# Kernel tuning notes

Hardware: AMD Instinct MI355X
Metric: run time of the kernel (lower is better)

The kernel has to match this reference:

```python
import jax, jax.numpy as jnp
import numpy as np

N, FEATS, CLASSES, E = 100000, 32, 16, 1600000
EMB_DIM = 1 + int(np.log2(FEATS))  # 6
HIDDEN = 3 + EMB_DIM               # 9
DEPTH = 10
DIFF = 0.9


def setup_inputs() -> dict:
    key = jax.random.key(0)
    ks = jax.random.split(key, 10)
    s = lambda k, *sh: jax.random.normal(k, sh, dtype=jnp.float32)
    return {
        "x": s(ks[0], N, FEATS),
        "edges": jax.random.randint(ks[1], (2, E), 0, N, dtype=jnp.int64),
        "emb_table": s(ks[2], FEATS, EMB_DIM) * 0.1,
        "W1": s(ks[3], 1 + EMB_DIM, HIDDEN) * 0.3,
        "b1": jnp.zeros((HIDDEN,), jnp.float32),
        "W2": s(ks[4], HIDDEN, 1) * 0.3,
        "b2": jnp.zeros((1,), jnp.float32),
        "Wout": s(ks[5], FEATS, CLASSES) * 0.1,
        "bout": jnp.zeros((CLASSES,), jnp.float32),
    }


def reference(x, edges, emb_table, W1, b1, W2, b2, Wout, bout):
    n, f = x.shape
    src, dst = edges[0], edges[1]
    # symmetric degree normalization (parameter-free GraphConv)
    deg = jax.ops.segment_sum(jnp.ones((src.shape[0],), x.dtype), dst, num_segments=n)
    deg = jnp.maximum(deg, 1.0)
    norm = jax.lax.rsqrt(deg[src] * deg[dst])  # [E]

    def conv(h):
        return jax.ops.segment_sum(h[src] * norm[:, None], dst, num_segments=n)

    def diffuse(h):
        h0 = h
        for _ in range(DEPTH):
            h = conv(h) * DIFF + (1.0 - DIFF) * h0
        return h

    x = diffuse(x)
    # per-(node, class) MLP: x.t().reshape(-1,1) orders rows class-major
    col = x.T.reshape(-1, 1)                       # [f*n, 1]
    emb = jnp.repeat(emb_table, n, axis=0)         # [f*n, EMB_DIM] (class cl repeated n times)
    h = jnp.concatenate([col, emb], axis=1)        # [f*n, 1+EMB_DIM]
    h = jax.nn.relu(h @ W1 + b1)
    h = h @ W2 + b2                                # [f*n, 1]
    x = h.reshape(f, n).T                          # [n, f]
    x = diffuse(x)
    return x @ Wout + bout
```

## Files before the change

### kernel.cpp

```cpp
#include <hip/hip_runtime.h>
#include <hip/hip_fp16.h>

#define ELL_CAP 64
#define NSLICE 8
#define EPB 2048


__global__ __launch_bounds__(256) void ell_fill(
    const int* __restrict__ edges, int* __restrict__ deg,
    int* __restrict__ ell, int e, int n, int slice_sz) {
    int slice = blockIdx.x & (NSLICE - 1);
    int chunk = blockIdx.x >> 3;
    int lo = slice * slice_sz;
    int hi = min(n, lo + slice_sz);
    int base = chunk * EPB + threadIdx.x;
#pragma unroll
    for (int k = 0; k < EPB / 256; ++k) {
        int i = base + k * 256;
        if (i >= e) break;
        int d = __builtin_nontemporal_load(&edges[e + i]);
        if (d < lo || d >= hi) continue;
        int s = __builtin_nontemporal_load(&edges[i]);
        int slot = atomicAdd(&deg[d], 1);
        if (slot < ELL_CAP) ell[((size_t)d << 6) + slot] = s;
    }
}

__global__ void nodeconst_kernel(const int* __restrict__ deg, float* __restrict__ rs,
                                 float* __restrict__ sq, float* __restrict__ wdeg,
                                 int* __restrict__ ell, int n) {
    int i = blockIdx.x * blockDim.x + threadIdx.x;
    if (i > n) return;
    int v = (i < n) ? deg[i] : 0;
    float d = (float)max(v, 1);
    float r = rsqrtf(d);
    rs[i] = r;
    sq[i] = sqrtf(d);
    wdeg[i] = 0.9f * r * r;
    if (i < n) {
        int dg = min(v, ELL_CAP);
        int dgp = (dg + 7) & ~7;
        for (int k = dg; k < dgp; ++k) ell[((size_t)i << 6) + k] = n;
    }
}

__global__ void prescale_kernel(const float2* __restrict__ x2, const float* __restrict__ rs,
                                __half2* __restrict__ g, int n) {
    int i = blockIdx.x * blockDim.x + threadIdx.x;
    int node = i >> 4;
    if (node > n) return;
    if (node == n) { g[i] = __floats2half2_rn(0.f, 0.f); return; }
    float2 v = x2[i];
    float r = rs[node];
    g[i] = __floats2half2_rn(v.x * r, v.y * r);
}


union H4 {
    uint2 u;
    __half2 h[2];
};

__global__ __launch_bounds__(256) void conv_kernel(
    const uint2* __restrict__ gin, const uint2* __restrict__ g0,
    uint2* __restrict__ gout, const int* __restrict__ deg,
    const int* __restrict__ ell, const float* __restrict__ wdeg, int n) {
    int gid = blockIdx.x * blockDim.x + threadIdx.x;
    int node = gid >> 3;
    int q = gid & 7;
    if (node > n) return;
    int dg = (node < n) ? min(deg[node], ELL_CAP) : 0;
    int dgp = (dg + 7) & ~7;
    int j0 = node << 6;
    int jend = j0 + dgp;
    float w = wdeg[node];
    H4 g0v;
    g0v.u = g0[gid];
    float ax0 = 0.f, ay0 = 0.f, az0 = 0.f, aw0 = 0.f;
    float ax1 = 0.f, ay1 = 0.f, az1 = 0.f, aw1 = 0.f;
    float ax2 = 0.f, ay2 = 0.f, az2 = 0.f, aw2 = 0.f;
    float ax3 = 0.f, ay3 = 0.f, az3 = 0.f, aw3 = 0.f;
    int scur = ell[j0 + q];
    for (int j = j0; j < jend; j += 8) {
        int snext = ell[j + 8 + q];
        int s0 = __shfl(scur, 0, 8), s1 = __shfl(scur, 1, 8);
        int s2 = __shfl(scur, 2, 8), s3 = __shfl(scur, 3, 8);
        int s4 = __shfl(scur, 4, 8), s5 = __shfl(scur, 5, 8);
        int s6 = __shfl(scur, 6, 8), s7 = __shfl(scur, 7, 8);
        H4 v0, v1, v2, v3, v4, v5, v6, v7;
        v0.u = gin[(size_t)s0 * 8 + q];
        v1.u = gin[(size_t)s1 * 8 + q];
        v2.u = gin[(size_t)s2 * 8 + q];
        v3.u = gin[(size_t)s3 * 8 + q];
        v4.u = gin[(size_t)s4 * 8 + q];
        v5.u = gin[(size_t)s5 * 8 + q];
        v6.u = gin[(size_t)s6 * 8 + q];
        v7.u = gin[(size_t)s7 * 8 + q];
        float2 lo, hi;
        lo = __half22float2(v0.h[0]); hi = __half22float2(v0.h[1]);
        ax0 += lo.x; ay0 += lo.y; az0 += hi.x; aw0 += hi.y;
        lo = __half22float2(v1.h[0]); hi = __half22float2(v1.h[1]);
        ax1 += lo.x; ay1 += lo.y; az1 += hi.x; aw1 += hi.y;
        lo = __half22float2(v2.h[0]); hi = __half22float2(v2.h[1]);
        ax2 += lo.x; ay2 += lo.y; az2 += hi.x; aw2 += hi.y;
        lo = __half22float2(v3.h[0]); hi = __half22float2(v3.h[1]);
        ax3 += lo.x; ay3 += lo.y; az3 += hi.x; aw3 += hi.y;
        lo = __half22float2(v4.h[0]); hi = __half22float2(v4.h[1]);
        ax0 += lo.x; ay0 += lo.y; az0 += hi.x; aw0 += hi.y;
        lo = __half22float2(v5.h[0]); hi = __half22float2(v5.h[1]);
        ax1 += lo.x; ay1 += lo.y; az1 += hi.x; aw1 += hi.y;
        lo = __half22float2(v6.h[0]); hi = __half22float2(v6.h[1]);
        ax2 += lo.x; ay2 += lo.y; az2 += hi.x; aw2 += hi.y;
        lo = __half22float2(v7.h[0]); hi = __half22float2(v7.h[1]);
        ax3 += lo.x; ay3 += lo.y; az3 += hi.x; aw3 += hi.y;
        scur = snext;
    }
    float2 g0lo = __half22float2(g0v.h[0]);
    float2 g0hi = __half22float2(g0v.h[1]);
    float rx = w * (ax0 + ax1 + ax2 + ax3) + 0.1f * g0lo.x;
    float ry = w * (ay0 + ay1 + ay2 + ay3) + 0.1f * g0lo.y;
    float rz = w * (az0 + az1 + az2 + az3) + 0.1f * g0hi.x;
    float rw = w * (aw0 + aw1 + aw2 + aw3) + 0.1f * g0hi.y;
    H4 o;
    o.h[0] = __floats2half2_rn(rx, ry);
    o.h[1] = __floats2half2_rn(rz, rw);
    gout[gid] = o.u;
}


__global__ __launch_bounds__(256) void mlp_kernel(
    const __half* __restrict__ gin, __half* __restrict__ gout,
    const float* __restrict__ rs, const float* __restrict__ sq,
    const float* __restrict__ emb,
    const float* __restrict__ W1,
    const float* __restrict__ b1,
    const float* __restrict__ W2,
    const float* __restrict__ b2,
    int n) {
    __shared__ float c[32][9];
    __shared__ float w0[9], w2[9];
    __shared__ float b2s;
    int tid = threadIdx.x;
    for (int i = tid; i < 288; i += blockDim.x) {
        int f = i / 9, jj = i % 9;
        float acc = b1[jj];
#pragma unroll
        for (int k = 0; k < 6; ++k) acc += emb[f * 6 + k] * W1[(1 + k) * 9 + jj];
        c[f][jj] = acc;
    }
    if (tid < 9) { w0[tid] = W1[tid]; w2[tid] = W2[tid]; }
    if (tid == 0) b2s = b2[0];
    __syncthreads();
    int gid = blockIdx.x * blockDim.x + tid;
    int node = gid >> 5;
    if (node > n) return;
    if (node == n) { gout[gid] = __float2half_rn(0.f); return; }
    int f = gid & 31;
    float xv = __half2float(gin[gid]) * sq[node];
    float acc = b2s;
#pragma unroll
    for (int jj = 0; jj < 9; ++jj)
        acc += fmaxf(xv * w0[jj] + c[f][jj], 0.0f) * w2[jj];
    gout[gid] = __float2half_rn(acc * rs[node]);
}


__global__ __launch_bounds__(256) void out_kernel(
    const __half* __restrict__ g, const float* __restrict__ sq,
    const float* __restrict__ Wout, const float* __restrict__ bout,
    float* __restrict__ out, int n) {
    __shared__ float w[32 * 16];
    __shared__ float bo[16];
    int tid = threadIdx.x;
    for (int i = tid; i < 512; i += blockDim.x) w[i] = Wout[i];
    if (tid < 16) bo[tid] = bout[tid];
    __syncthreads();
    int gid = blockIdx.x * blockDim.x + tid;
    int node = gid >> 4;
    int cls = gid & 15;
    if (node >= n) return;
    const __half* gr = g + (size_t)node * 32;
    float acc = 0.0f;
#pragma unroll
    for (int f = 0; f < 32; ++f) acc += __half2float(gr[f]) * w[f * 16 + cls];
    out[gid] = acc * sq[node] + bo[cls];
}

extern "C" void kernel_launch(void* const* d_in, const int* in_sizes, int n_in,
                              void* d_out, int out_size, void* d_ws, size_t ws_size,
                              hipStream_t stream) {
    const float* x    = (const float*)d_in[0];
    const int* edges  = (const int*)d_in[1];
    const float* emb  = (const float*)d_in[2];
    const float* W1   = (const float*)d_in[3];
    const float* b1   = (const float*)d_in[4];
    const float* W2   = (const float*)d_in[5];
    const float* b2   = (const float*)d_in[6];
    const float* Wout = (const float*)d_in[7];
    const float* bout = (const float*)d_in[8];
    float* out        = (float*)d_out;

    const int N = in_sizes[0] / 32;
    const int E = in_sizes[1] / 2;

    size_t off = 0;
    auto walloc = [&](size_t bytes) {
        void* p = (char*)d_ws + off;
        off += (bytes + 255) & ~(size_t)255;
        return p;
    };
    int*     deg   = (int*)    walloc((size_t)(N + 1) * 4);
    float*   rs    = (float*)  walloc((size_t)(N + 1) * 4);
    float*   sq    = (float*)  walloc((size_t)(N + 1) * 4);
    float*   wdeg  = (float*)  walloc((size_t)(N + 1) * 4);
    int*     ell   = (int*)    walloc((size_t)(N + 1) * ELL_CAP * 4 + 256);
    __half*  g0buf = (__half*) walloc((size_t)(N + 1) * 32 * 2);
    __half*  bufA  = (__half*) walloc((size_t)(N + 1) * 32 * 2);
    __half*  bufB  = (__half*) walloc((size_t)(N + 1) * 32 * 2);

    hipMemsetAsync(deg, 0, (size_t)(N + 1) * 4, stream);
    {
        int slice_sz = (N + NSLICE - 1) / NSLICE;
        int chunks = (E + EPB - 1) / EPB;
        ell_fill<<<chunks * NSLICE, 256, 0, stream>>>(edges, deg, ell, E, N, slice_sz);
    }
    nodeconst_kernel<<<(N + 1 + 255) / 256, 256, 0, stream>>>(deg, rs, sq, wdeg, ell, N);

    const int conv_blocks = ((N + 1) * 8 + 255) / 256;
    const int elem_blocks = ((N + 1) * 32 + 255) / 256;
    const int pair_blocks = ((N + 1) * 16 + 255) / 256;

    prescale_kernel<<<pair_blocks, 256, 0, stream>>>((const float2*)x, rs,
                                                     (__half2*)g0buf, N);

    {
        const uint2* gin = (const uint2*)g0buf;
        for (int it = 0; it < 10; ++it) {
            uint2* go = (uint2*)((it & 1) ? bufB : bufA);
            conv_kernel<<<conv_blocks, 256, 0, stream>>>(gin, (const uint2*)g0buf, go,
                                                         deg, ell, wdeg, N);
            gin = go;
        }
    }
    mlp_kernel<<<elem_blocks, 256, 0, stream>>>(bufB, g0buf, rs, sq, emb, W1, b1, W2, b2, N);

    {
        const uint2* gin = (const uint2*)g0buf;
        for (int it = 0; it < 10; ++it) {
            uint2* go = (uint2*)((it & 1) ? bufB : bufA);
            conv_kernel<<<conv_blocks, 256, 0, stream>>>(gin, (const uint2*)g0buf, go,
                                                         deg, ell, wdeg, N);
            gin = go;
        }
    }
    out_kernel<<<(N * 16 + 255) / 256, 256, 0, stream>>>(bufB, sq, Wout, bout, out, N);
}
```

Measured before the change: 639.1 us.

## Split feature buffers into two 16-feature planes for cache-local gathers

```diff
diff --git a/kernel.cpp b/kernel.cpp
--- a/kernel.cpp
+++ b/kernel.cpp
@@ -44,87 +44,76 @@
     }
 }
 
+
 __global__ void prescale_kernel(const float2* __restrict__ x2, const float* __restrict__ rs,
                                 __half2* __restrict__ g, int n) {
     int i = blockIdx.x * blockDim.x + threadIdx.x;
     int node = i >> 4;
     if (node > n) return;
-    if (node == n) { g[i] = __floats2half2_rn(0.f, 0.f); return; }
+    int j = i & 15;
+    int plane = j >> 3;
+    size_t ps8 = (size_t)(n + 1) * 8;
+    size_t a = (size_t)plane * ps8 + (size_t)node * 8 + (j & 7);
+    if (node == n) { g[a] = __floats2half2_rn(0.f, 0.f); return; }
     float2 v = x2[i];
     float r = rs[node];
-    g[i] = __floats2half2_rn(v.x * r, v.y * r);
-}
-
-
-union H4 {
-    uint2 u;
-    __half2 h[2];
-};
+    g[a] = __floats2half2_rn(v.x * r, v.y * r);
+}
+
 
 __global__ __launch_bounds__(256) void conv_kernel(
-    const uint2* __restrict__ gin, const uint2* __restrict__ g0,
-    uint2* __restrict__ gout, const int* __restrict__ deg,
+    const unsigned* __restrict__ gin, const unsigned* __restrict__ g0,
+    unsigned* __restrict__ gout, const int* __restrict__ deg,
     const int* __restrict__ ell, const float* __restrict__ wdeg, int n) {
-    int gid = blockIdx.x * blockDim.x + threadIdx.x;
-    int node = gid >> 3;
-    int q = gid & 7;
+    int half = blockIdx.x & 1;
+    int lid = (blockIdx.x >> 1) * blockDim.x + threadIdx.x;
+    int node = lid >> 3;
+    int q = lid & 7;
     if (node > n) return;
+    size_t ps = (size_t)(n + 1) * 8;
+    const unsigned* gp = gin + (size_t)half * ps;
     int dg = (node < n) ? min(deg[node], ELL_CAP) : 0;
-    int dgp = (dg + 7) & ~7;
+    int trips = (dg + 7) >> 3;
     int j0 = node << 6;
-    int jend = j0 + dgp;
     float w = wdeg[node];
-    H4 g0v;
-    g0v.u = g0[gid];
-    float ax0 = 0.f, ay0 = 0.f, az0 = 0.f, aw0 = 0.f;
-    float ax1 = 0.f, ay1 = 0.f, az1 = 0.f, aw1 = 0.f;
-    float ax2 = 0.f, ay2 = 0.f, az2 = 0.f, aw2 = 0.f;
-    float ax3 = 0.f, ay3 = 0.f, az3 = 0.f, aw3 = 0.f;
+    size_t oidx = (size_t)half * ps + ((size_t)node << 3) + q;
+    union UH { unsigned u; __half2 h; };
+    UH g0v;
+    g0v.u = g0[oidx];
+    float2 a0 = {0.f, 0.f}, a1 = {0.f, 0.f}, a2 = {0.f, 0.f}, a3 = {0.f, 0.f};
     int scur = ell[j0 + q];
-    for (int j = j0; j < jend; j += 8) {
-        int snext = ell[j + 8 + q];
+    for (int r = 0; r < trips; ++r) {
+        int snext = ell[j0 + (r + 1) * 8 + q];
         int s0 = __shfl(scur, 0, 8), s1 = __shfl(scur, 1, 8);
         int s2 = __shfl(scur, 2, 8), s3 = __shfl(scur, 3, 8);
         int s4 = __shfl(scur, 4, 8), s5 = __shfl(scur, 5, 8);
         int s6 = __shfl(scur, 6, 8), s7 = __shfl(scur, 7, 8);
-        H4 v0, v1, v2, v3, v4, v5, v6, v7;
-        v0.u = gin[(size_t)s0 * 8 + q];
-        v1.u = gin[(size_t)s1 * 8 + q];
-        v2.u = gin[(size_t)s2 * 8 + q];
-        v3.u = gin[(size_t)s3 * 8 + q];
-        v4.u = gin[(size_t)s4 * 8 + q];
-        v5.u = gin[(size_t)s5 * 8 + q];
-        v6.u = gin[(size_t)s6 * 8 + q];
-        v7.u = gin[(size_t)s7 * 8 + q];
-        float2 lo, hi;
-        lo = __half22float2(v0.h[0]); hi = __half22float2(v0.h[1]);
-        ax0 += lo.x; ay0 += lo.y; az0 += hi.x; aw0 += hi.y;
-        lo = __half22float2(v1.h[0]); hi = __half22float2(v1.h[1]);
-        ax1 += lo.x; ay1 += lo.y; az1 += hi.x; aw1 += hi.y;
-        lo = __half22float2(v2.h[0]); hi = __half22float2(v2.h[1]);
-        ax2 += lo.x; ay2 += lo.y; az2 += hi.x; aw2 += hi.y;
-        lo = __half22float2(v3.h[0]); hi = __half22float2(v3.h[1]);
-        ax3 += lo.x; ay3 += lo.y; az3 += hi.x; aw3 += hi.y;
-        lo = __half22float2(v4.h[0]); hi = __half22float2(v4.h[1]);
-        ax0 += lo.x; ay0 += lo.y; az0 += hi.x; aw0 += hi.y;
-        lo = __half22float2(v5.h[0]); hi = __half22float2(v5.h[1]);
-        ax1 += lo.x; ay1 += lo.y; az1 += hi.x; aw1 += hi.y;
-        lo = __half22float2(v6.h[0]); hi = __half22float2(v6.h[1]);
-        ax2 += lo.x; ay2 += lo.y; az2 += hi.x; aw2 += hi.y;
-        lo = __half22float2(v7.h[0]); hi = __half22float2(v7.h[1]);
-        ax3 += lo.x; ay3 += lo.y; az3 += hi.x; aw3 += hi.y;
+        UH v0, v1, v2, v3, v4, v5, v6, v7;
+        v0.u = gp[(size_t)s0 * 8 + q];
+        v1.u = gp[(size_t)s1 * 8 + q];
+        v2.u = gp[(size_t)s2 * 8 + q];
+        v3.u = gp[(size_t)s3 * 8 + q];
+        v4.u = gp[(size_t)s4 * 8 + q];
+        v5.u = gp[(size_t)s5 * 8 + q];
+        v6.u = gp[(size_t)s6 * 8 + q];
+        v7.u = gp[(size_t)s7 * 8 + q];
+        float2 t;
+        t = __half22float2(v0.h); a0.x += t.x; a0.y += t.y;
+        t = __half22float2(v1.h); a1.x += t.x; a1.y += t.y;
+        t = __half22float2(v2.h); a2.x += t.x; a2.y += t.y;
+        t = __half22float2(v3.h); a3.x += t.x; a3.y += t.y;
+        t = __half22float2(v4.h); a0.x += t.x; a0.y += t.y;
+        t = __half22float2(v5.h); a1.x += t.x; a1.y += t.y;
+        t = __half22float2(v6.h); a2.x += t.x; a2.y += t.y;
+        t = __half22float2(v7.h); a3.x += t.x; a3.y += t.y;
         scur = snext;
     }
-    float2 g0lo = __half22float2(g0v.h[0]);
-    float2 g0hi = __half22float2(g0v.h[1]);
-    float rx = w * (ax0 + ax1 + ax2 + ax3) + 0.1f * g0lo.x;
-    float ry = w * (ay0 + ay1 + ay2 + ay3) + 0.1f * g0lo.y;
-    float rz = w * (az0 + az1 + az2 + az3) + 0.1f * g0hi.x;
-    float rw = w * (aw0 + aw1 + aw2 + aw3) + 0.1f * g0hi.y;
-    H4 o;
-    o.h[0] = __floats2half2_rn(rx, ry);
-    o.h[1] = __floats2half2_rn(rz, rw);
-    gout[gid] = o.u;
+    float2 g0f = __half22float2(g0v.h);
+    float rx = w * (a0.x + a1.x + a2.x + a3.x) + 0.1f * g0f.x;
+    float ry = w * (a0.y + a1.y + a2.y + a3.y) + 0.1f * g0f.y;
+    UH o;
+    o.h = __floats2half2_rn(rx, ry);
+    gout[oidx] = o.u;
 }
 
 
@@ -154,14 +143,16 @@
     int gid = blockIdx.x * blockDim.x + tid;
     int node = gid >> 5;
     if (node > n) return;
-    if (node == n) { gout[gid] = __float2half_rn(0.f); return; }
     int f = gid & 31;
-    float xv = __half2float(gin[gid]) * sq[node];
+    size_t ps16 = (size_t)(n + 1) * 16;
+    size_t a = (size_t)(f >> 4) * ps16 + (size_t)node * 16 + (f & 15);
+    if (node == n) { gout[a] = __float2half_rn(0.f); return; }
+    float xv = __half2float(gin[a]) * sq[node];
     float acc = b2s;
 #pragma unroll
     for (int jj = 0; jj < 9; ++jj)
         acc += fmaxf(xv * w0[jj] + c[f][jj], 0.0f) * w2[jj];
-    gout[gid] = __float2half_rn(acc * rs[node]);
+    gout[a] = __float2half_rn(acc * rs[node]);
 }
 
 
@@ -179,10 +170,14 @@
     int node = gid >> 4;
     int cls = gid & 15;
     if (node >= n) return;
-    const __half* gr = g + (size_t)node * 32;
+    size_t ps16 = (size_t)(n + 1) * 16;
+    const __half* g0p = g + (size_t)node * 16;
+    const __half* g1p = g + ps16 + (size_t)node * 16;
     float acc = 0.0f;
 #pragma unroll
-    for (int f = 0; f < 32; ++f) acc += __half2float(gr[f]) * w[f * 16 + cls];
+    for (int f = 0; f < 16; ++f) acc += __half2float(g0p[f]) * w[f * 16 + cls];
+#pragma unroll
+    for (int f = 0; f < 16; ++f) acc += __half2float(g1p[f]) * w[(16 + f) * 16 + cls];
     out[gid] = acc * sq[node] + bo[cls];
 }
 
@@ -226,7 +221,8 @@
     }
     nodeconst_kernel<<<(N + 1 + 255) / 256, 256, 0, stream>>>(deg, rs, sq, wdeg, ell, N);
 
-    const int conv_blocks = ((N + 1) * 8 + 255) / 256;
+    const int blocks_per_half = ((N + 1) * 8 + 255) / 256;
+    const int conv_blocks = blocks_per_half * 2;
     const int elem_blocks = ((N + 1) * 32 + 255) / 256;
     const int pair_blocks = ((N + 1) * 16 + 255) / 256;
 
@@ -234,10 +230,10 @@
                                                      (__half2*)g0buf, N);
 
     {
-        const uint2* gin = (const uint2*)g0buf;
+        const unsigned* gin = (const unsigned*)g0buf;
         for (int it = 0; it < 10; ++it) {
-            uint2* go = (uint2*)((it & 1) ? bufB : bufA);
-            conv_kernel<<<conv_blocks, 256, 0, stream>>>(gin, (const uint2*)g0buf, go,
+            unsigned* go = (unsigned*)((it & 1) ? bufB : bufA);
+            conv_kernel<<<conv_blocks, 256, 0, stream>>>(gin, (const unsigned*)g0buf, go,
                                                          deg, ell, wdeg, N);
             gin = go;
         }
@@ -245,10 +241,10 @@
     mlp_kernel<<<elem_blocks, 256, 0, stream>>>(bufB, g0buf, rs, sq, emb, W1, b1, W2, b2, N);
 
     {
-        const uint2* gin = (const uint2*)g0buf;
+        const unsigned* gin = (const unsigned*)g0buf;
         for (int it = 0; it < 10; ++it) {
-            uint2* go = (uint2*)((it & 1) ? bufB : bufA);
-            conv_kernel<<<conv_blocks, 256, 0, stream>>>(gin, (const uint2*)g0buf, go,
+            unsigned* go = (unsigned*)((it & 1) ? bufB : bufA);
+            conv_kernel<<<conv_blocks, 256, 0, stream>>>(gin, (const unsigned*)g0buf, go,
                                                          deg, ell, wdeg, N);
             gin = go;
         }
```

Result: slower. 677.0 us (+5.9%).
